# Kernel optimization log

Measured on AMD Instinct MI355X. Metric: run time of the kernel, lower is better.

The kernel has to match this reference:

```python
import jax, jax.numpy as jnp
import numpy as np

B, S, D = 4, 2048, 1024
H = 16
HD = D // H
PF = 4096
EPS = 1e-5


def setup_inputs() -> dict:
    key = jax.random.key(0)
    ks = jax.random.split(key, 16)
    s = 1.0 / np.sqrt(D)
    inp = {
        'src': jax.random.normal(ks[0], (B, S, D), jnp.float32),
        'Wq': jax.random.normal(ks[1], (D, D), jnp.float32) * s,
        'bq': jnp.zeros((D,), jnp.float32),
        'Wk': jax.random.normal(ks[2], (D, D), jnp.float32) * s,
        'bk': jnp.zeros((D,), jnp.float32),
        'Wv': jax.random.normal(ks[3], (D, D), jnp.float32) * s,
        'bv': jnp.zeros((D,), jnp.float32),
        'Wo': jax.random.normal(ks[4], (D, D), jnp.float32) * s,
        'bo': jnp.zeros((D,), jnp.float32),
        'g1': jnp.ones((D,), jnp.float32),
        'b1': jnp.zeros((D,), jnp.float32),
        'W1': jax.random.normal(ks[5], (D, PF), jnp.float32) * s,
        'bf1': jnp.zeros((PF,), jnp.float32),
        'W2': jax.random.normal(ks[6], (PF, D), jnp.float32) * (1.0 / np.sqrt(PF)),
        'bf2': jnp.zeros((D,), jnp.float32),
        'g2': jnp.ones((D,), jnp.float32),
        'b2': jnp.zeros((D,), jnp.float32),
    }
    return inp


def _layer_norm(x, g, b):
    mu = jnp.mean(x, axis=-1, keepdims=True)
    var = jnp.mean(jnp.square(x - mu), axis=-1, keepdims=True)
    return (x - mu) * jax.lax.rsqrt(var + EPS) * g + b


def reference(src, Wq, bq, Wk, bk, Wv, bv, Wo, bo, g1, b1, W1, bf1, W2, bf2, g2, b2):
    scale = 1.0 / np.sqrt(HD)
    # QKV projections -> [B, H, S, HD]
    q = (src @ Wq + bq).reshape(B, S, H, HD).transpose(0, 2, 1, 3)
    k = (src @ Wk + bk).reshape(B, S, H, HD).transpose(0, 2, 1, 3)
    v = (src @ Wv + bv).reshape(B, S, H, HD).transpose(0, 2, 1, 3)
    # attention scores [B, H, S, S]
    attn = jax.nn.softmax(jnp.einsum('bhqd,bhkd->bhqk', q, k) * scale, axis=-1)
    x = jnp.einsum('bhqk,bhkd->bhqd', attn, v)
    x = x.transpose(0, 2, 1, 3).reshape(B, S, D)
    attn_out = x @ Wo + bo
    # residual + LN (dropout is identity at p=0)
    src1 = _layer_norm(src + attn_out, g1, b1)
    # positionwise FFN: Linear -> Dropout -> ReLU -> Linear
    ff = jax.nn.relu(src1 @ W1 + bf1) @ W2 + bf2
    return _layer_norm(src1 + ff, g2, b2)
```

## Files before the change

kernel.cpp:

```cpp
#include <hip/hip_runtime.h>

#define BB 4
#define SS 2048
#define DD 1024
#define HH 16
#define PFF 4096
#define MR 8192

typedef unsigned short u16;
typedef __attribute__((ext_vector_type(8))) short s16x8;
typedef __attribute__((ext_vector_type(4))) float f32x4v;
typedef __attribute__((ext_vector_type(4))) unsigned short u16x4;
typedef __attribute__((ext_vector_type(8))) unsigned short u16x8;

__device__ inline u16 f2bf(float f) {
  union { float f; unsigned u; } v; v.f = f;
  unsigned r = v.u + 0x7FFFu + ((v.u >> 16) & 1u);
  return (u16)(r >> 16);
}

__device__ inline unsigned cvtpk_bf16(float lo, float hi) {
  unsigned r;
  asm("v_cvt_pk_bf16_f32 %0, %1, %2" : "=v"(r) : "v"(lo), "v"(hi));
  return r;
}

__device__ inline void gload16(const void* g, void* l) {
  __builtin_amdgcn_global_load_lds(
      (const __attribute__((address_space(1))) void*)g,
      (__attribute__((address_space(3))) void*)l, 16, 0, 0);
}

__device__ inline f32x4v MFMA(s16x8 a, s16x8 b, f32x4v c) {
  return __builtin_amdgcn_mfma_f32_16x16x32_bf16(a, b, c, 0, 0, 0);
}

#define RAWBAR()                          \
  do {                                    \
    asm volatile("" ::: "memory");        \
    __builtin_amdgcn_s_barrier();         \
    asm volatile("" ::: "memory");        \
  } while (0)
#define WAITVM(N) asm volatile("s_waitcnt vmcnt(" #N ")" ::: "memory")

__device__ inline s16x8 ldfrag(const u16* base, int row, int colByte) {
  return *(const s16x8*)((const char*)base + row * 128 + (colByte ^ ((row & 7) << 4)));
}

template <int RELU, int OUTBF>
__global__ __launch_bounds__(512, 1) void gemm256(
    const u16* __restrict__ A, const u16* __restrict__ Bt,
    const float* __restrict__ bias, float* __restrict__ Cf,
    u16* __restrict__ Cb, int M, int N, int K, int ntx) {
  __shared__ __align__(128) u16 lds[3 * 16384];
  const int t = threadIdx.x;
  const int lane = t & 63, w = t >> 6;
  const int wr = w >> 2, wc = w & 3;
  const int g = lane >> 4, q = lane & 15;

  const int cpx = gridDim.x >> 3;
  const int wg = (blockIdx.x & 7) * cpx + (blockIdx.x >> 3);
  const int row0 = (wg / ntx) * 256, col0 = (wg % ntx) * 256;

  f32x4v acc[8][4];
#pragma unroll
  for (int m = 0; m < 8; ++m)
#pragma unroll
    for (int n = 0; n < 4; ++n) acc[m][n] = (f32x4v){0.f, 0.f, 0.f, 0.f};

  const int sr0 = t >> 2, sc0 = (t & 3) * 8;
  const int sr1 = (t + 512) >> 2;
  const u16* Ag0 = A + (size_t)(row0 + sr0) * K + sc0;
  const u16* Ag1 = A + (size_t)(row0 + sr1) * K + sc0;
  const u16* Bg0 = Bt + (size_t)(col0 + sr0) * K + sc0;
  const u16* Bg1 = Bt + (size_t)(col0 + sr1) * K + sc0;
  const int wud = (t & ~63) * 8;

#define STAGE_A(kt, buf)                                          \
  do {                                                            \
    u16* ab_ = &lds[(buf) * 16384];                               \
    gload16(Ag0 + (kt) * 32, ab_ + wud);                          \
    gload16(Ag1 + (kt) * 32, ab_ + 4096 + wud);                   \
  } while (0)
#define STAGE_B(kt, buf)                                          \
  do {                                                            \
    u16* bb_ = &lds[(buf) * 16384 + 8192];                        \
    gload16(Bg0 + (kt) * 32, bb_ + wud);                          \
    gload16(Bg1 + (kt) * 32, bb_ + 4096 + wud);                   \
  } while (0)

  const int NT = K / 32;
  STAGE_A(0, 0); STAGE_B(0, 0);
  STAGE_A(1, 1); STAGE_B(1, 1);
  WAITVM(4);
  RAWBAR();

  int cur = 0, nxt = 2;
  for (int kt = 0; kt < NT; ++kt) {
    const u16* ab = &lds[cur * 16384];
    const u16* bb = ab + 8192;
    const bool pf = (kt + 2 < NT);
    if (pf) STAGE_A(kt + 2, nxt);
    s16x8 bf_[4], af_[4];
#pragma unroll
    for (int n = 0; n < 4; ++n)
      bf_[n] = *(const s16x8*)&bb[(wc * 64 + n * 16 + q) * 32 + g * 8];
#pragma unroll
    for (int m = 0; m < 4; ++m)
      af_[m] = *(const s16x8*)&ab[(wr * 128 + m * 16 + q) * 32 + g * 8];
    RAWBAR();
    __builtin_amdgcn_s_setprio(1);
#pragma unroll
    for (int m = 0; m < 4; ++m)
#pragma unroll
      for (int n = 0; n < 4; ++n) acc[m][n] = MFMA(af_[m], bf_[n], acc[m][n]);
    __builtin_amdgcn_s_setprio(0);
    RAWBAR();
    if (pf) STAGE_B(kt + 2, nxt);
#pragma unroll
    for (int m = 0; m < 4; ++m)
      af_[m] = *(const s16x8*)&ab[(wr * 128 + (m + 4) * 16 + q) * 32 + g * 8];
    RAWBAR();
    __builtin_amdgcn_s_setprio(1);
#pragma unroll
    for (int m = 0; m < 4; ++m)
#pragma unroll
      for (int n = 0; n < 4; ++n) acc[m + 4][n] = MFMA(af_[m], bf_[n], acc[m + 4][n]);
    __builtin_amdgcn_s_setprio(0);
    if (kt + 1 < NT) {
      if (pf) WAITVM(4);
      else WAITVM(0);
    }
    RAWBAR();
    cur = (cur == 2) ? 0 : cur + 1;
    nxt = (nxt == 2) ? 0 : nxt + 1;
  }
#undef STAGE_A
#undef STAGE_B

#pragma unroll
  for (int n = 0; n < 4; ++n) {
    const int col = col0 + wc * 64 + 16 * n + q;
    const float bv = bias[col];
#pragma unroll
    for (int m = 0; m < 8; ++m) {
#pragma unroll
      for (int r = 0; r < 4; ++r) {
        const int row = row0 + wr * 128 + 16 * m + 4 * g + r;
        float v = acc[m][n][r] + bv;
        if (RELU) v = fmaxf(v, 0.f);
        if (OUTBF) Cb[(size_t)row * N + col] = f2bf(v);
        else Cf[(size_t)row * N + col] = v;
      }
    }
  }
}

template <int RELU, int OUTBF>
__global__ __launch_bounds__(256) void gemm_bf16(
    const u16* __restrict__ A, const u16* __restrict__ Bt,
    const float* __restrict__ bias, float* __restrict__ Cf,
    u16* __restrict__ Cb, int M, int N, int K) {
  __shared__ __align__(128) u16 As[128 * 32];
  __shared__ __align__(128) u16 Bs[128 * 32];
  const int t = threadIdx.x;
  const int lane = t & 63, w = t >> 6;
  const int wr = w >> 1, wc = w & 1;
  const int g = lane >> 4, q = lane & 15;
  const int row0 = blockIdx.y * 128, col0 = blockIdx.x * 128;

  f32x4v acc[4][4];
#pragma unroll
  for (int m = 0; m < 4; ++m)
#pragma unroll
    for (int n = 0; n < 4; ++n) acc[m][n] = (f32x4v){0.f, 0.f, 0.f, 0.f};

  const int c0 = t, c1 = 256 + t;
  const int ar0 = c0 >> 2, ac0 = (c0 & 3) * 8;
  const int ar1 = c1 >> 2, ac1 = (c1 & 3) * 8;
  const u16* Ar0 = A + (size_t)(row0 + ar0) * K + ac0;
  const u16* Ar1 = A + (size_t)(row0 + ar1) * K + ac1;
  const u16* Br0 = Bt + (size_t)(col0 + ar0) * K + ac0;
  const u16* Br1 = Bt + (size_t)(col0 + ar1) * K + ac1;
  char* AsB = (char*)As;
  char* BsB = (char*)Bs;
  const int ldst = (t & ~63) * 16;

  for (int k0 = 0; k0 < K; k0 += 32) {
    __syncthreads();
    gload16(Ar0 + k0, AsB + ldst);
    gload16(Ar1 + k0, AsB + 4096 + ldst);
    gload16(Br0 + k0, BsB + ldst);
    gload16(Br1 + k0, BsB + 4096 + ldst);
    __syncthreads();
    s16x8 af[4], bfr[4];
#pragma unroll
    for (int m = 0; m < 4; ++m)
      af[m] = *(const s16x8*)&As[(wr * 64 + 16 * m + q) * 32 + g * 8];
#pragma unroll
    for (int n = 0; n < 4; ++n)
      bfr[n] = *(const s16x8*)&Bs[(wc * 64 + 16 * n + q) * 32 + g * 8];
#pragma unroll
    for (int m = 0; m < 4; ++m)
#pragma unroll
      for (int n = 0; n < 4; ++n) acc[m][n] = MFMA(af[m], bfr[n], acc[m][n]);
  }
#pragma unroll
  for (int n = 0; n < 4; ++n) {
    const int col = col0 + wc * 64 + 16 * n + q;
    const float bv = bias[col];
#pragma unroll
    for (int m = 0; m < 4; ++m) {
#pragma unroll
      for (int r = 0; r < 4; ++r) {
        const int row = row0 + wr * 64 + 16 * m + 4 * g + r;
        float v = acc[m][n][r] + bv;
        if (RELU) v = fmaxf(v, 0.f);
        if (OUTBF) Cb[(size_t)row * N + col] = f2bf(v);
        else Cf[(size_t)row * N + col] = v;
      }
    }
  }
}

__global__ __launch_bounds__(256) void attn_mfma(
    const u16* __restrict__ qkv, const u16* __restrict__ vt,
    u16* __restrict__ xb) {
  __shared__ __align__(128) u16 Qs[64 * 64];
  __shared__ __align__(128) u16 Ks[2][64 * 64];
  __shared__ __align__(128) u16 Vs[2][64 * 64];
  __shared__ __align__(128) u16 Ps[4][16 * 64];

  const int t = threadIdx.x;
  const int w = t >> 6, lane = t & 63;
  const int g = lane >> 4, q = lane & 15;
  const int bh = blockIdx.y, b = bh >> 4, h = bh & 15;
  const int q0 = blockIdx.x * 64;
  const int qcol = h * 64, kcol = DD + h * 64;
  const int ldst = (t & ~63) * 16;

  const int r0 = t >> 3, c0e = ((t & 7) ^ (r0 & 7)) * 8;
  const int r1 = (t + 256) >> 3, c1e = ((t & 7) ^ (r1 & 7)) * 8;
  const u16* Ksrc0 = qkv + (size_t)(b * SS + r0) * 3072 + kcol + c0e;
  const u16* Ksrc1 = qkv + (size_t)(b * SS + r1) * 3072 + kcol + c1e;
  const u16* Vsrc0 = vt + (size_t)(bh * 64 + r0) * SS + c0e;
  const u16* Vsrc1 = vt + (size_t)(bh * 64 + r1) * SS + c1e;

  gload16(qkv + (size_t)(b * SS + q0 + r0) * 3072 + qcol + c0e, (char*)Qs + ldst);
  gload16(qkv + (size_t)(b * SS + q0 + r1) * 3072 + qcol + c1e, (char*)Qs + 4096 + ldst);
  gload16(Ksrc0, (char*)Ks[0] + ldst);
  gload16(Ksrc1, (char*)Ks[0] + 4096 + ldst);
  gload16(Vsrc0, (char*)Vs[0] + ldst);
  gload16(Vsrc1, (char*)Vs[0] + 4096 + ldst);
  WAITVM(0);
  RAWBAR();

  const s16x8 bq0 = ldfrag(Qs, w * 16 + q, g * 16);
  const s16x8 bq1 = ldfrag(Qs, w * 16 + q, 64 + g * 16);

  float m_run = -1e30f, l_run = 0.f;
  f32x4v oacc[4];
#pragma unroll
  for (int n = 0; n < 4; ++n) oacc[n] = (f32x4v){0.f, 0.f, 0.f, 0.f};
  const float SCL2 = 0.18033688011112042f;

  u16* Pw = Ps[w];
  uint2* pdst[4];
#pragma unroll
  for (int m = 0; m < 4; ++m)
    pdst[m] = (uint2*)((char*)Pw + q * 128 + ((32 * m + 8 * g) ^ ((q & 7) << 4)));

  for (int kt = 0; kt < SS / 64; ++kt) {
    const int cur = kt & 1;
    if (kt < SS / 64 - 1) {
      const size_t koff = (size_t)(kt + 1) * 64 * 3072;
      const int voff = (kt + 1) * 64;
      gload16(Ksrc0 + koff, (char*)Ks[cur ^ 1] + ldst);
      gload16(Ksrc1 + koff, (char*)Ks[cur ^ 1] + 4096 + ldst);
      gload16(Vsrc0 + voff, (char*)Vs[cur ^ 1] + ldst);
      gload16(Vsrc1 + voff, (char*)Vs[cur ^ 1] + 4096 + ldst);
    }

    f32x4v sacc[4];
    __builtin_amdgcn_s_setprio(1);
#pragma unroll
    for (int m = 0; m < 4; ++m) {
      sacc[m] = (f32x4v){0.f, 0.f, 0.f, 0.f};
      s16x8 a0 = ldfrag(Ks[cur], 16 * m + q, g * 16);
      s16x8 a1 = ldfrag(Ks[cur], 16 * m + q, 64 + g * 16);
      sacc[m] = MFMA(a0, bq0, sacc[m]);
      sacc[m] = MFMA(a1, bq1, sacc[m]);
    }
    __builtin_amdgcn_s_setprio(0);

    float sc[16];
    float tm = -1e30f;
#pragma unroll
    for (int m = 0; m < 4; ++m)
#pragma unroll
      for (int r = 0; r < 4; ++r) {
        float sv = sacc[m][r] * SCL2;
        sc[m * 4 + r] = sv;
        tm = fmaxf(tm, sv);
      }
    tm = fmaxf(tm, __shfl_xor(tm, 16));
    tm = fmaxf(tm, __shfl_xor(tm, 32));
    if (!__all(tm <= m_run + 8.f)) {
      const float m_new = fmaxf(m_run, tm);
      const float rf = exp2f(m_run - m_new);
      float rfo[4];
#pragma unroll
      for (int r = 0; r < 4; ++r) rfo[r] = __shfl(rf, 4 * g + r);
#pragma unroll
      for (int n = 0; n < 4; ++n) {
        oacc[n][0] *= rfo[0]; oacc[n][1] *= rfo[1];
        oacc[n][2] *= rfo[2]; oacc[n][3] *= rfo[3];
      }
      l_run *= rf;
      m_run = m_new;
    }
    float psum = 0.f;
#pragma unroll
    for (int m = 0; m < 4; ++m) {
      float p0 = exp2f(sc[m * 4 + 0] - m_run);
      float p1 = exp2f(sc[m * 4 + 1] - m_run);
      float p2 = exp2f(sc[m * 4 + 2] - m_run);
      float p3 = exp2f(sc[m * 4 + 3] - m_run);
      psum += (p0 + p1) + (p2 + p3);
      uint2 pw;
      pw.x = cvtpk_bf16(p0, p1);
      pw.y = cvtpk_bf16(p2, p3);
      *pdst[m] = pw;
    }
    psum += __shfl_xor(psum, 16);
    psum += __shfl_xor(psum, 32);
    l_run += psum;

    __builtin_amdgcn_s_setprio(1);
#pragma unroll
    for (int s = 0; s < 2; ++s) {
      s16x8 ap = ldfrag(Pw, q, s * 64 + g * 16);
#pragma unroll
      for (int n = 0; n < 4; ++n) {
        s16x8 bv = ldfrag(Vs[cur], 16 * n + q, s * 64 + g * 16);
        oacc[n] = MFMA(ap, bv, oacc[n]);
      }
    }
    __builtin_amdgcn_s_setprio(0);

    if (kt < SS / 64 - 1) WAITVM(0);
    RAWBAR();
  }

  const float invl = 1.f / l_run;
  float invo[4];
#pragma unroll
  for (int r = 0; r < 4; ++r) invo[r] = __shfl(invl, 4 * g + r);
#pragma unroll
  for (int n = 0; n < 4; ++n)
#pragma unroll
    for (int r = 0; r < 4; ++r) {
      const size_t row = (size_t)(b * SS + q0 + w * 16 + 4 * g + r);
      xb[row * DD + h * 64 + 16 * n + q] = f2bf(oacc[n][r] * invo[r]);
    }
}

__global__ __launch_bounds__(256) void cvt_bf16(const float* __restrict__ x,
                                                u16* __restrict__ y, int n4) {
  int i = blockIdx.x * 256 + threadIdx.x;
  if (i < n4) {
    float4 v = ((const float4*)x)[i];
    u16x4 o;
    o[0] = f2bf(v.x); o[1] = f2bf(v.y); o[2] = f2bf(v.z); o[3] = f2bf(v.w);
    ((u16x4*)y)[i] = o;
  }
}

__global__ __launch_bounds__(256) void transpose_w(const float* __restrict__ W,
                                                   u16* __restrict__ Wt,
                                                   int K, int N) {
  __shared__ float T[32][33];
  const int n0 = blockIdx.x * 32, k0 = blockIdx.y * 32;
  const int t = threadIdx.x;
  const int r = t >> 3, c = (t & 7) * 4;
  float4 v = *(const float4*)&W[(size_t)(k0 + r) * N + n0 + c];
  T[r][c] = v.x; T[r][c + 1] = v.y; T[r][c + 2] = v.z; T[r][c + 3] = v.w;
  __syncthreads();
  const int a = t >> 3, b0 = (t & 7) * 4;
  u16x4 o;
#pragma unroll
  for (int j = 0; j < 4; ++j) o[j] = f2bf(T[b0 + j][a]);
  *(u16x4*)&Wt[(size_t)(n0 + a) * K + k0 + b0] = o;
}

__global__ __launch_bounds__(256) void vtrans(const u16* __restrict__ qkv,
                                              u16* __restrict__ vt) {
  __shared__ u16 T[64 * 72];
  const int t = threadIdx.x;
  const int bh = blockIdx.y, b = bh >> 4, h = bh & 15;
  const int s0 = blockIdx.x * 64;
  const int vcol = 2048 + h * 64;
#pragma unroll
  for (int i = 0; i < 2; ++i) {
    int c = i * 256 + t;
    int sr = c >> 3, dc = (c & 7) * 8;
    *(u16x8*)&T[sr * 72 + dc] =
        *(const u16x8*)&qkv[(size_t)(b * SS + s0 + sr) * 3072 + vcol + dc];
  }
  __syncthreads();
#pragma unroll
  for (int i = 0; i < 2; ++i) {
    int c = i * 256 + t;
    int d = c >> 3, scnk = (c & 7) * 8;
    u16x8 o;
#pragma unroll
    for (int j = 0; j < 8; ++j) o[j] = T[(scnk + j) * 72 + d];
    *(u16x8*)&vt[(size_t)(bh * 64 + d) * SS + s0 + scnk] = o;
  }
}

__global__ __launch_bounds__(256) void concat3(const float* __restrict__ a,
                                               const float* __restrict__ b,
                                               const float* __restrict__ c,
                                               float* __restrict__ o) {
  int i = blockIdx.x * 256 + threadIdx.x;
  if (i < 3072)
    o[i] = i < 1024 ? a[i] : (i < 2048 ? b[i - 1024] : c[i - 2048]);
}

template <int WB>
__global__ __launch_bounds__(256) void ln_res(
    const float* __restrict__ X, const float* __restrict__ R,
    const float* __restrict__ g, const float* __restrict__ b,
    float* __restrict__ Y, u16* __restrict__ Yb) {
  const int row = blockIdx.x;
  const int t = threadIdx.x;
  const size_t off = (size_t)row * DD + t * 4;

  float4 x4 = *(const float4*)&X[off];
  float4 r4 = *(const float4*)&R[off];
  float v0 = x4.x + r4.x, v1 = x4.y + r4.y, v2 = x4.z + r4.z, v3 = x4.w + r4.w;

  float s1 = v0 + v1 + v2 + v3;
  float s2 = v0 * v0 + v1 * v1 + v2 * v2 + v3 * v3;
#pragma unroll
  for (int o = 1; o < 64; o <<= 1) {
    s1 += __shfl_xor(s1, o);
    s2 += __shfl_xor(s2, o);
  }
  __shared__ float red1[4], red2[4];
  if ((t & 63) == 0) {
    red1[t >> 6] = s1;
    red2[t >> 6] = s2;
  }
  __syncthreads();
  s1 = red1[0] + red1[1] + red1[2] + red1[3];
  s2 = red2[0] + red2[1] + red2[2] + red2[3];

  const float mu = s1 * (1.f / DD);
  const float var = s2 * (1.f / DD) - mu * mu;
  const float rs = rsqrtf(var + 1e-5f);

  float4 g4 = *(const float4*)&g[t * 4];
  float4 b4 = *(const float4*)&b[t * 4];
  float4 y;
  y.x = (v0 - mu) * rs * g4.x + b4.x;
  y.y = (v1 - mu) * rs * g4.y + b4.y;
  y.z = (v2 - mu) * rs * g4.z + b4.z;
  y.w = (v3 - mu) * rs * g4.w + b4.w;
  *(float4*)&Y[off] = y;
  if (WB) {
    u16x4 o;
    o[0] = f2bf(y.x); o[1] = f2bf(y.y); o[2] = f2bf(y.z); o[3] = f2bf(y.w);
    *(u16x4*)&Yb[off] = o;
  }
}

extern "C" void kernel_launch(void* const* d_in, const int* in_sizes, int n_in,
                              void* d_out, int out_size, void* d_ws,
                              size_t ws_size, hipStream_t stream) {
  const float* src = (const float*)d_in[0];
  const float* Wq  = (const float*)d_in[1];
  const float* bq  = (const float*)d_in[2];
  const float* Wk  = (const float*)d_in[3];
  const float* bk  = (const float*)d_in[4];
  const float* Wv  = (const float*)d_in[5];
  const float* bv  = (const float*)d_in[6];
  const float* Wo  = (const float*)d_in[7];
  const float* bo  = (const float*)d_in[8];
  const float* g1  = (const float*)d_in[9];
  const float* b1  = (const float*)d_in[10];
  const float* W1  = (const float*)d_in[11];
  const float* bf1 = (const float*)d_in[12];
  const float* W2  = (const float*)d_in[13];
  const float* bf2 = (const float*)d_in[14];
  const float* g2  = (const float*)d_in[15];
  const float* b2  = (const float*)d_in[16];

  char* W = (char*)d_ws;
  u16*   wqkvT = (u16*)  (W + 0);
  u16*   woT   = (u16*)  (W + 6291456);
  u16*   w1T   = (u16*)  (W + 8388608);
  u16*   w2T   = (u16*)  (W + 16777216);
  float* bqkv  = (float*)(W + 25165824);
  u16*   srcb  = (u16*)  (W + 25178112);
  u16*   qkv   = (u16*)  (W + 41955328);
  u16*   vt    = (u16*)  (W + 92286976);
  u16*   xb    = (u16*)  (W + 109064192);
  float* pb    = (float*)(W + 125841408);
  float* s1f   = (float*)(W + 159395840);
  u16*   s1bb  = (u16*)  (W + 109064192);
  u16*   f1b   = (u16*)  (W + 41955328);
  float* f2b   = (float*)(W + 125841408);

  dim3 blk(256);

  cvt_bf16<<<8192, blk, 0, stream>>>(src, srcb, MR * DD / 4);
  transpose_w<<<dim3(32, 32), blk, 0, stream>>>(Wq, wqkvT, DD, DD);
  transpose_w<<<dim3(32, 32), blk, 0, stream>>>(Wk, wqkvT + (size_t)1024 * 1024, DD, DD);
  transpose_w<<<dim3(32, 32), blk, 0, stream>>>(Wv, wqkvT + (size_t)2048 * 1024, DD, DD);
  transpose_w<<<dim3(32, 32), blk, 0, stream>>>(Wo, woT, DD, DD);
  transpose_w<<<dim3(128, 32), blk, 0, stream>>>(W1, w1T, DD, PFF);
  transpose_w<<<dim3(32, 128), blk, 0, stream>>>(W2, w2T, PFF, DD);
  concat3<<<12, blk, 0, stream>>>(bq, bk, bv, bqkv);

  gemm256<0, 1><<<384, 512, 0, stream>>>(srcb, wqkvT, bqkv, nullptr, qkv,
                                         MR, 3072, DD, 12);
  vtrans<<<dim3(32, 64), blk, 0, stream>>>(qkv, vt);
  attn_mfma<<<dim3(32, 64), blk, 0, stream>>>(qkv, vt, xb);
  gemm_bf16<0, 0><<<dim3(8, 64), blk, 0, stream>>>(xb, woT, bo, pb, nullptr,
                                                   MR, DD, DD);
  ln_res<1><<<MR, blk, 0, stream>>>(src, pb, g1, b1, s1f, s1bb);
  gemm256<1, 1><<<512, 512, 0, stream>>>(s1bb, w1T, bf1, nullptr, f1b,
                                         MR, PFF, DD, 16);
  gemm_bf16<0, 0><<<dim3(8, 64), blk, 0, stream>>>(f1b, w2T, bf2, f2b, nullptr,
                                                   MR, DD, PFF);
  ln_res<0><<<MR, blk, 0, stream>>>(s1f, f2b, g2, b2, (float*)d_out, nullptr);
}
```

Before: 534.2 us.

## Rewrite attention with 32x32 MFMA, register-resident P, and 256-row query tiles

The attention kernel now uses 32x32x16 bf16 MFMA and computes S^T so each lane owns one query row. That removes the cross-lane max/sum shuffles and the per-row rescale broadcasts. P stays in registers via v_permlane32_swap instead of round-tripping through LDS. Each 512-thread block covers 256 query rows, so every K/V tile loaded is shared by eight waves, and blocks are remapped so heads interleave across the grid. The cost is higher register pressure from two 16-wide accumulators per lane and reliance on the permlane swap instruction.

```diff
diff --git a/kernel.cpp b/kernel.cpp
--- a/kernel.cpp
+++ b/kernel.cpp
@@ -10,6 +10,7 @@
 typedef unsigned short u16;
 typedef __attribute__((ext_vector_type(8))) short s16x8;
 typedef __attribute__((ext_vector_type(4))) float f32x4v;
+typedef __attribute__((ext_vector_type(16))) float f32x16;
 typedef __attribute__((ext_vector_type(4))) unsigned short u16x4;
 typedef __attribute__((ext_vector_type(8))) unsigned short u16x8;
 
@@ -33,6 +34,9 @@
 
 __device__ inline f32x4v MFMA(s16x8 a, s16x8 b, f32x4v c) {
   return __builtin_amdgcn_mfma_f32_16x16x32_bf16(a, b, c, 0, 0, 0);
+}
+__device__ inline f32x16 MFMA32(s16x8 a, s16x8 b, f32x16 c) {
+  return __builtin_amdgcn_mfma_f32_32x32x16_bf16(a, b, c, 0, 0, 0);
 }
 
 #define RAWBAR()                          \
@@ -223,146 +227,149 @@
   }
 }
 
-__global__ __launch_bounds__(256) void attn_mfma(
+__global__ __launch_bounds__(512, 4) void attn_mfma(
     const u16* __restrict__ qkv, const u16* __restrict__ vt,
     u16* __restrict__ xb) {
-  __shared__ __align__(128) u16 Qs[64 * 64];
-  __shared__ __align__(128) u16 Ks[2][64 * 64];
-  __shared__ __align__(128) u16 Vs[2][64 * 64];
-  __shared__ __align__(128) u16 Ps[4][16 * 64];
+  __shared__ __align__(128) u16 lds[16384];
 
   const int t = threadIdx.x;
   const int w = t >> 6, lane = t & 63;
-  const int g = lane >> 4, q = lane & 15;
-  const int bh = blockIdx.y, b = bh >> 4, h = bh & 15;
-  const int q0 = blockIdx.x * 64;
+  const int q = lane & 31, hi = lane >> 5;
+
+  const int flat = blockIdx.x;
+  const int j = flat >> 3;
+  const int bh = (flat & 7) * 8 + (j & 7);
+  const int qb = j >> 3;
+  const int b = bh >> 4, h = bh & 15;
+  const int q0 = qb * 256;
   const int qcol = h * 64, kcol = DD + h * 64;
+
+  const int sr = t >> 3;
+  const int sc = ((t & 7) ^ (sr & 7)) * 8;
   const int ldst = (t & ~63) * 16;
-
-  const int r0 = t >> 3, c0e = ((t & 7) ^ (r0 & 7)) * 8;
-  const int r1 = (t + 256) >> 3, c1e = ((t & 7) ^ (r1 & 7)) * 8;
-  const u16* Ksrc0 = qkv + (size_t)(b * SS + r0) * 3072 + kcol + c0e;
-  const u16* Ksrc1 = qkv + (size_t)(b * SS + r1) * 3072 + kcol + c1e;
-  const u16* Vsrc0 = vt + (size_t)(bh * 64 + r0) * SS + c0e;
-  const u16* Vsrc1 = vt + (size_t)(bh * 64 + r1) * SS + c1e;
-
-  gload16(qkv + (size_t)(b * SS + q0 + r0) * 3072 + qcol + c0e, (char*)Qs + ldst);
-  gload16(qkv + (size_t)(b * SS + q0 + r1) * 3072 + qcol + c1e, (char*)Qs + 4096 + ldst);
-  gload16(Ksrc0, (char*)Ks[0] + ldst);
-  gload16(Ksrc1, (char*)Ks[0] + 4096 + ldst);
-  gload16(Vsrc0, (char*)Vs[0] + ldst);
-  gload16(Vsrc1, (char*)Vs[0] + 4096 + ldst);
+  const u16* Ksrc = qkv + (size_t)(b * SS + sr) * 3072 + kcol + sc;
+  const u16* Vsrc = vt + (size_t)(bh * 64 + sr) * SS + sc;
+
+  {
+    const u16* Qsrc = qkv + (size_t)(b * SS + q0 + sr) * 3072 + qcol + sc;
+#pragma unroll
+    for (int jj = 0; jj < 4; ++jj)
+      gload16(Qsrc + (size_t)jj * 64 * 3072, (char*)lds + jj * 8192 + ldst);
+  }
   WAITVM(0);
   RAWBAR();
-
-  const s16x8 bq0 = ldfrag(Qs, w * 16 + q, g * 16);
-  const s16x8 bq1 = ldfrag(Qs, w * 16 + q, 64 + g * 16);
+  s16x8 qf[4];
+  {
+    const u16* Qw = lds + w * 2048;
+#pragma unroll
+    for (int s = 0; s < 4; ++s) qf[s] = ldfrag(Qw, q, 32 * s + 16 * hi);
+  }
+  asm volatile("s_waitcnt lgkmcnt(0)" ::: "memory");
+  __builtin_amdgcn_sched_barrier(0);
+  RAWBAR();
+
+  gload16(Ksrc, (char*)lds + ldst);
+  gload16(Vsrc, (char*)lds + 8192 + ldst);
+  WAITVM(0);
+  RAWBAR();
 
   float m_run = -1e30f, l_run = 0.f;
-  f32x4v oacc[4];
-#pragma unroll
-  for (int n = 0; n < 4; ++n) oacc[n] = (f32x4v){0.f, 0.f, 0.f, 0.f};
+  f32x16 oac0, oac1;
+#pragma unroll
+  for (int i = 0; i < 16; ++i) { oac0[i] = 0.f; oac1[i] = 0.f; }
   const float SCL2 = 0.18033688011112042f;
-
-  u16* Pw = Ps[w];
-  uint2* pdst[4];
-#pragma unroll
-  for (int m = 0; m < 4; ++m)
-    pdst[m] = (uint2*)((char*)Pw + q * 128 + ((32 * m + 8 * g) ^ ((q & 7) << 4)));
 
   for (int kt = 0; kt < SS / 64; ++kt) {
     const int cur = kt & 1;
-    if (kt < SS / 64 - 1) {
-      const size_t koff = (size_t)(kt + 1) * 64 * 3072;
-      const int voff = (kt + 1) * 64;
-      gload16(Ksrc0 + koff, (char*)Ks[cur ^ 1] + ldst);
-      gload16(Ksrc1 + koff, (char*)Ks[cur ^ 1] + 4096 + ldst);
-      gload16(Vsrc0 + voff, (char*)Vs[cur ^ 1] + ldst);
-      gload16(Vsrc1 + voff, (char*)Vs[cur ^ 1] + 4096 + ldst);
-    }
-
-    f32x4v sacc[4];
+    const u16* Kc = lds + cur * 8192;
+    const u16* Vc = Kc + 4096;
+    if (kt + 1 < SS / 64) {
+      const size_t ko = (size_t)(kt + 1) * 64 * 3072;
+      const int vo = (kt + 1) * 64;
+      gload16(Ksrc + ko, (char*)lds + (cur ^ 1) * 16384 + ldst);
+      gload16(Vsrc + vo, (char*)lds + (cur ^ 1) * 16384 + 8192 + ldst);
+    }
+
+    f32x16 sa0, sa1;
+#pragma unroll
+    for (int i = 0; i < 16; ++i) { sa0[i] = 0.f; sa1[i] = 0.f; }
     __builtin_amdgcn_s_setprio(1);
 #pragma unroll
-    for (int m = 0; m < 4; ++m) {
-      sacc[m] = (f32x4v){0.f, 0.f, 0.f, 0.f};
-      s16x8 a0 = ldfrag(Ks[cur], 16 * m + q, g * 16);
-      s16x8 a1 = ldfrag(Ks[cur], 16 * m + q, 64 + g * 16);
-      sacc[m] = MFMA(a0, bq0, sacc[m]);
-      sacc[m] = MFMA(a1, bq1, sacc[m]);
+    for (int s = 0; s < 4; ++s) {
+      s16x8 k0 = ldfrag(Kc, q, 32 * s + 16 * hi);
+      s16x8 k1 = ldfrag(Kc, 32 + q, 32 * s + 16 * hi);
+      sa0 = MFMA32(k0, qf[s], sa0);
+      sa1 = MFMA32(k1, qf[s], sa1);
     }
     __builtin_amdgcn_s_setprio(0);
 
-    float sc[16];
-    float tm = -1e30f;
-#pragma unroll
-    for (int m = 0; m < 4; ++m)
-#pragma unroll
-      for (int r = 0; r < 4; ++r) {
-        float sv = sacc[m][r] * SCL2;
-        sc[m * 4 + r] = sv;
-        tm = fmaxf(tm, sv);
-      }
-    tm = fmaxf(tm, __shfl_xor(tm, 16));
+    float tm = fmaxf(sa0[0], sa1[0]);
+#pragma unroll
+    for (int i = 1; i < 16; ++i) tm = fmaxf(tm, fmaxf(sa0[i], sa1[i]));
+    tm *= SCL2;
     tm = fmaxf(tm, __shfl_xor(tm, 32));
     if (!__all(tm <= m_run + 8.f)) {
       const float m_new = fmaxf(m_run, tm);
       const float rf = exp2f(m_run - m_new);
-      float rfo[4];
-#pragma unroll
-      for (int r = 0; r < 4; ++r) rfo[r] = __shfl(rf, 4 * g + r);
-#pragma unroll
-      for (int n = 0; n < 4; ++n) {
-        oacc[n][0] *= rfo[0]; oacc[n][1] *= rfo[1];
-        oacc[n][2] *= rfo[2]; oacc[n][3] *= rfo[3];
-      }
+#pragma unroll
+      for (int i = 0; i < 16; ++i) { oac0[i] *= rf; oac1[i] *= rf; }
       l_run *= rf;
       m_run = m_new;
     }
     float psum = 0.f;
 #pragma unroll
-    for (int m = 0; m < 4; ++m) {
-      float p0 = exp2f(sc[m * 4 + 0] - m_run);
-      float p1 = exp2f(sc[m * 4 + 1] - m_run);
-      float p2 = exp2f(sc[m * 4 + 2] - m_run);
-      float p3 = exp2f(sc[m * 4 + 3] - m_run);
-      psum += (p0 + p1) + (p2 + p3);
-      uint2 pw;
-      pw.x = cvtpk_bf16(p0, p1);
-      pw.y = cvtpk_bf16(p2, p3);
-      *pdst[m] = pw;
-    }
-    psum += __shfl_xor(psum, 16);
+    for (int i = 0; i < 16; ++i) {
+      sa0[i] = exp2f(fmaf(sa0[i], SCL2, -m_run));
+      sa1[i] = exp2f(fmaf(sa1[i], SCL2, -m_run));
+      psum += sa0[i] + sa1[i];
+    }
     psum += __shfl_xor(psum, 32);
     l_run += psum;
 
     __builtin_amdgcn_s_setprio(1);
 #pragma unroll
-    for (int s = 0; s < 2; ++s) {
-      s16x8 ap = ldfrag(Pw, q, s * 64 + g * 16);
-#pragma unroll
-      for (int n = 0; n < 4; ++n) {
-        s16x8 bv = ldfrag(Vs[cur], 16 * n + q, s * 64 + g * 16);
-        oacc[n] = MFMA(ap, bv, oacc[n]);
+    for (int s = 0; s < 4; ++s) {
+      const int rb = 8 * (s & 1);
+      float p0, p1, p2, p3, p4, p5, p6, p7;
+      if (s < 2) {
+        p0 = sa0[rb]; p1 = sa0[rb + 1]; p2 = sa0[rb + 2]; p3 = sa0[rb + 3];
+        p4 = sa0[rb + 4]; p5 = sa0[rb + 5]; p6 = sa0[rb + 6]; p7 = sa0[rb + 7];
+      } else {
+        p0 = sa1[rb]; p1 = sa1[rb + 1]; p2 = sa1[rb + 2]; p3 = sa1[rb + 3];
+        p4 = sa1[rb + 4]; p5 = sa1[rb + 5]; p6 = sa1[rb + 6]; p7 = sa1[rb + 7];
       }
+      unsigned a0 = cvtpk_bf16(p0, p1);
+      unsigned a1 = cvtpk_bf16(p2, p3);
+      unsigned b0 = cvtpk_bf16(p4, p5);
+      unsigned b1 = cvtpk_bf16(p6, p7);
+      asm("v_permlane32_swap_b32 %0, %1" : "+v"(a0), "+v"(b0));
+      asm("v_permlane32_swap_b32 %0, %1" : "+v"(a1), "+v"(b1));
+      union { unsigned u[4]; s16x8 v; } pf;
+      pf.u[0] = a0; pf.u[1] = a1; pf.u[2] = b0; pf.u[3] = b1;
+      s16x8 v0 = ldfrag(Vc, q, 32 * s + 16 * hi);
+      s16x8 v1 = ldfrag(Vc, 32 + q, 32 * s + 16 * hi);
+      oac0 = MFMA32(v0, pf.v, oac0);
+      oac1 = MFMA32(v1, pf.v, oac1);
     }
     __builtin_amdgcn_s_setprio(0);
 
-    if (kt < SS / 64 - 1) WAITVM(0);
+    WAITVM(0);
     RAWBAR();
   }
 
-  const float invl = 1.f / l_run;
-  float invo[4];
-#pragma unroll
-  for (int r = 0; r < 4; ++r) invo[r] = __shfl(invl, 4 * g + r);
-#pragma unroll
-  for (int n = 0; n < 4; ++n)
-#pragma unroll
-    for (int r = 0; r < 4; ++r) {
-      const size_t row = (size_t)(b * SS + q0 + w * 16 + 4 * g + r);
-      xb[row * DD + h * 64 + 16 * n + q] = f2bf(oacc[n][r] * invo[r]);
-    }
+  const float inv = 1.f / l_run;
+  const size_t row = (size_t)(b * SS + q0 + w * 32 + q);
+  u16* orow = xb + row * DD + qcol;
+#pragma unroll
+  for (int rr = 0; rr < 4; ++rr) {
+    uint2 pw0, pw1;
+    pw0.x = cvtpk_bf16(oac0[4 * rr] * inv, oac0[4 * rr + 1] * inv);
+    pw0.y = cvtpk_bf16(oac0[4 * rr + 2] * inv, oac0[4 * rr + 3] * inv);
+    pw1.x = cvtpk_bf16(oac1[4 * rr] * inv, oac1[4 * rr + 1] * inv);
+    pw1.y = cvtpk_bf16(oac1[4 * rr + 2] * inv, oac1[4 * rr + 3] * inv);
+    *(uint2*)(orow + 8 * rr + 4 * hi) = pw0;
+    *(uint2*)(orow + 32 + 8 * rr + 4 * hi) = pw1;
+  }
 }
 
 __global__ __launch_bounds__(256) void cvt_bf16(const float* __restrict__ x,
@@ -414,7 +421,7 @@
     int d = c >> 3, scnk = (c & 7) * 8;
     u16x8 o;
 #pragma unroll
-    for (int j = 0; j < 8; ++j) o[j] = T[(scnk + j) * 72 + d];
+    for (int jj = 0; jj < 8; ++jj) o[jj] = T[(scnk + jj) * 72 + d];
     *(u16x8*)&vt[(size_t)(bh * 64 + d) * SS + s0 + scnk] = o;
   }
 }
@@ -527,7 +534,7 @@
   gemm256<0, 1><<<384, 512, 0, stream>>>(srcb, wqkvT, bqkv, nullptr, qkv,
                                          MR, 3072, DD, 12);
   vtrans<<<dim3(32, 64), blk, 0, stream>>>(qkv, vt);
-  attn_mfma<<<dim3(32, 64), blk, 0, stream>>>(qkv, vt, xb);
+  attn_mfma<<<512, 512, 0, stream>>>(qkv, vt, xb);
   gemm_bf16<0, 0><<<dim3(8, 64), blk, 0, stream>>>(xb, woT, bo, pb, nullptr,
                                                    MR, DD, DD);
   ln_res<1><<<MR, blk, 0, stream>>>(src, pb, g1, b1, s1f, s1bb);
```

Result: faster. 488.9 us (-8.5%).
